# Kernel optimization log

Measured on AMD Instinct MI355X. Metric: run time of the kernel, lower is better.

Reference implementation:

```python
import jax, jax.numpy as jnp
import numpy as np

N_NODES = 50000
N_EDGES = 800000
IN_FEATS = 128
HIDDEN = 128
NUM_CLASSES = 47


def setup_inputs() -> dict:
    key = jax.random.key(0)
    k1, k2, k3, k4 = jax.random.split(key, 4)
    features = jax.random.normal(k1, (N_NODES, IN_FEATS), dtype=jnp.float32)
    edge_index = jax.random.randint(k2, (2, N_EDGES), 0, N_NODES, dtype=jnp.int32)
    # Glorot-style init for weights, zeros for bias (DGL GraphConv defaults)
    W1 = jax.random.normal(k3, (IN_FEATS, HIDDEN), dtype=jnp.float32) * (1.0 / np.sqrt(IN_FEATS))
    b1 = jnp.zeros((HIDDEN,), dtype=jnp.float32)
    W2 = jax.random.normal(k4, (HIDDEN, NUM_CLASSES), dtype=jnp.float32) * (1.0 / np.sqrt(HIDDEN))
    b2 = jnp.zeros((NUM_CLASSES,), dtype=jnp.float32)
    return {"features": features, "edge_index": edge_index,
            "W1": W1, "b1": b1, "W2": W2, "b2": b2}


def _graph_conv(x, W, b, src, dst, norm_src, norm_dst, n_nodes):
    # DGL GraphConv, norm='both': D_dst^{-1/2} A D_src^{-1/2} (X W) + b
    h = (x * norm_src[:, None]) @ W            # transform before aggregation
    agg = jax.ops.segment_sum(h[src], dst, num_segments=n_nodes)
    return agg * norm_dst[:, None] + b


def reference(features, edge_index, W1, b1, W2, b2):
    src, dst = edge_index[0], edge_index[1]
    n = features.shape[0]
    ones = jnp.ones((src.shape[0],), dtype=features.dtype)
    deg_out = jax.ops.segment_sum(ones, src, num_segments=n)
    deg_in = jax.ops.segment_sum(ones, dst, num_segments=n)
    norm_src = jax.lax.rsqrt(jnp.clip(deg_out, 1.0))   # d_out^{-1/2}, clamp >= 1
    norm_dst = jax.lax.rsqrt(jnp.clip(deg_in, 1.0))    # d_in^{-1/2}, clamp >= 1

    h = _graph_conv(features, W1, b1, src, dst, norm_src, norm_dst, n)
    h = jax.nn.relu(h)
    out = _graph_conv(h, W2, b2, src, dst, norm_src, norm_dst, n)
    return out
```

## Files before the change

kernel.cpp:

```cpp
#include <hip/hip_runtime.h>
#include <hip/hip_fp16.h>

#define N_NODES 50000
#define N_EDGES 800000
#define IN_F 128
#define HID 128
#define NCLS 47
#define H2S 48
#define W2C 64
#define NCH 196
#define NB 128
#define CHUNK 6250
#define SB 16
#define SCHUNK 50000
#define PDW 12500
#define G1B 196
#define G1ROWS 256
#define G2ROWS 128


typedef _Float16 f16x8 __attribute__((ext_vector_type(8)));
typedef float f32x4 __attribute__((ext_vector_type(4)));

struct __align__(8)  h2x2 { __half2 a, b; };
struct __align__(16) h2x4 { __half2 a, b, c, d; };

__global__ __launch_bounds__(256) void prep_kernel(const float* __restrict__ W1,
                                                   const float* __restrict__ W2,
                                                   __half* __restrict__ W1Th,
                                                   __half* __restrict__ W1Tl,
                                                   __half* __restrict__ W2Th,
                                                   __half* __restrict__ W2Tl) {
    const int b = blockIdx.x, t = threadIdx.x;
    if (b < 32) {
        const int i0 = b * 512;
        for (int i2 = i0 + t; i2 < i0 + 512; i2 += 256) {
            int cc = i2 >> 7, k = i2 & 127;
            float w = W1[k * HID + cc];
            __half hv = __float2half_rn(w);
            W1Th[i2] = hv;
            W1Tl[i2] = __float2half_rn(w - __half2float(hv));
        }
    } else {
        const int i0 = (b - 32) * 512;
        for (int i2 = i0 + t; i2 < i0 + 512; i2 += 256) {
            int cc = i2 >> 7, k = i2 & 127;
            float w = (cc < NCLS) ? W2[k * NCLS + cc] : 0.f;
            __half hv = __float2half_rn(w);
            W2Th[i2] = hv;
            W2Tl[i2] = __float2half_rn(w - __half2float(hv));
        }
    }
}

__global__ __launch_bounds__(512) void hist_gemm1_kernel(const int* __restrict__ ei,
        unsigned int* __restrict__ Pdst, unsigned int* __restrict__ Psrc,
        const float* __restrict__ X, const __half* __restrict__ W1Th,
        const __half* __restrict__ W1Tl, __half* __restrict__ H1h) {
    __shared__ unsigned int h[PDW];
    const int t = threadIdx.x;
    if (blockIdx.x >= G1B) {
        const int hb = blockIdx.x - G1B;
        const bool is_src = hb >= NB;
        const int chunk = is_src ? (hb - NB) : hb;
        const int* ids = is_src ? ei : ei + N_EDGES;
        const int cnt = is_src ? SCHUNK : CHUNK;
        uint2* h2 = (uint2*)h;
        for (int j = t; j < PDW / 2; j += 512) h2[j] = make_uint2(0u, 0u);
        __syncthreads();
        const int e0 = chunk * cnt;
        const int2* e2p = (const int2*)(ids + e0);
        for (int k = t; k < cnt / 2; k += 512) {
            int2 v2 = e2p[k];
            atomicAdd(&h[v2.x >> 2], 1u << ((v2.x & 3) * 8));
            atomicAdd(&h[v2.y >> 2], 1u << ((v2.y & 3) * 8));
        }
        __syncthreads();
        unsigned int* P = (is_src ? Psrc : Pdst) + (size_t)chunk * PDW;
        uint2* P2 = (uint2*)P;
        for (int j = t; j < PDW / 2; j += 512) P2[j] = h2[j];
    } else {
        const int lane = t & 63;
        const int wv = t >> 6;
        const int r16 = lane & 15;
        const int kg = lane >> 4;
        const int row0 = blockIdx.x * G1ROWS + wv * 32;
        f32x4 acc[2][8] = {};
#pragma unroll
        for (int s = 0; s < 4; ++s) {
            const int k0 = 32 * s + 8 * kg;
            f16x8 ah[2], al[2];
#pragma unroll
            for (int rt = 0; rt < 2; ++rt) {
                int row = row0 + rt * 16 + r16;
                int rc = row < N_NODES ? row : N_NODES - 1;
                const float4 x0 = *(const float4*)&X[(size_t)rc * IN_F + k0];
                const float4 x1 = *(const float4*)&X[(size_t)rc * IN_F + k0 + 4];
                const float xv[8] = {x0.x, x0.y, x0.z, x0.w,
                                     x1.x, x1.y, x1.z, x1.w};
#pragma unroll
                for (int j = 0; j < 8; ++j) {
                    _Float16 hv = (_Float16)xv[j];
                    ah[rt][j] = hv;
                    al[rt][j] = (_Float16)(xv[j] - (float)hv);
                }
            }
#pragma unroll
            for (int tt = 0; tt < 8; ++tt) {
                const f16x8 bh = *(const f16x8*)&W1Th[(16 * tt + r16) * IN_F + k0];
                const f16x8 bl = *(const f16x8*)&W1Tl[(16 * tt + r16) * IN_F + k0];
#pragma unroll
                for (int rt = 0; rt < 2; ++rt) {
                    acc[rt][tt] = __builtin_amdgcn_mfma_f32_16x16x32_f16(
                        ah[rt], bh, acc[rt][tt], 0, 0, 0);
                    acc[rt][tt] = __builtin_amdgcn_mfma_f32_16x16x32_f16(
                        al[rt], bh, acc[rt][tt], 0, 0, 0);
                    acc[rt][tt] = __builtin_amdgcn_mfma_f32_16x16x32_f16(
                        ah[rt], bl, acc[rt][tt], 0, 0, 0);
                }
            }
        }
#pragma unroll
        for (int rt = 0; rt < 2; ++rt)
#pragma unroll
            for (int j = 0; j < 4; ++j) {
                const int row = row0 + rt * 16 + 4 * kg + j;
                if (row < N_NODES) {
#pragma unroll
                    for (int tt = 0; tt < 8; ++tt)
                        H1h[(size_t)row * HID + 16 * tt + r16] =
                            __float2half_rn(acc[rt][tt][j]);
                }
            }
    }
}

__global__ __launch_bounds__(256) void reduce_kernel(unsigned int* __restrict__ Pdst,
                                                     const unsigned int* __restrict__ Psrc,
                                                     int* __restrict__ cnt_in,
                                                     float* __restrict__ norm_src,
                                                     float* __restrict__ norm_dst,
                                                     int* __restrict__ chunk_sums) {
    __shared__ int sm[256];
    const int t = threadIdx.x;
    const int j = blockIdx.x * 256 + t;
    int tot = 0;
    if (j < PDW) {
        unsigned int run = 0;
#pragma unroll 8
        for (int b = 0; b < NB; ++b) {
            unsigned int v = Pdst[(size_t)b * PDW + j];
            Pdst[(size_t)b * PDW + j] = run;
            run += v;
        }
        int n0 = run & 0xff, n1 = (run >> 8) & 0xff;
        int n2 = (run >> 16) & 0xff, n3 = (run >> 24) & 0xff;
        *(int4*)&cnt_in[4 * j] = make_int4(n0, n1, n2, n3);
        *(float4*)&norm_dst[4 * j] = make_float4(
            rsqrtf(fmaxf((float)n0, 1.0f)), rsqrtf(fmaxf((float)n1, 1.0f)),
            rsqrtf(fmaxf((float)n2, 1.0f)), rsqrtf(fmaxf((float)n3, 1.0f)));
        tot = n0 + n1 + n2 + n3;
        unsigned int rs = 0;
#pragma unroll
        for (int b = 0; b < SB; ++b) rs += Psrc[(size_t)b * PDW + j];
        int s0 = rs & 0xff, s1 = (rs >> 8) & 0xff;
        int s2 = (rs >> 16) & 0xff, s3 = (rs >> 24) & 0xff;
        *(float4*)&norm_src[4 * j] = make_float4(
            rsqrtf(fmaxf((float)s0, 1.0f)), rsqrtf(fmaxf((float)s1, 1.0f)),
            rsqrtf(fmaxf((float)s2, 1.0f)), rsqrtf(fmaxf((float)s3, 1.0f)));
    }
    sm[t] = tot;
    __syncthreads();
    const int g = t & 63;
    for (int off = 32; off > 0; off >>= 1) {
        if (g < off) sm[t] += sm[t + off];
        __syncthreads();
    }
    if (g == 0) chunk_sums[blockIdx.x * 4 + (t >> 6)] = sm[t];
}

__global__ __launch_bounds__(256) void scan3_kernel(const int* __restrict__ cnt_in,
                                                    const int* __restrict__ chunk_sums,
                                                    int* __restrict__ offsets) {
    __shared__ int sm[256];
    const int t = threadIdx.x;
    int v = (t < NCH) ? chunk_sums[t] : 0;
    sm[t] = v;
    __syncthreads();
    for (int off = 1; off < 256; off <<= 1) {
        int u = (t >= off) ? sm[t - off] : 0;
        __syncthreads();
        sm[t] += u;
        __syncthreads();
    }
    const int basev = (blockIdx.x == 0) ? 0 : sm[blockIdx.x - 1];
    __syncthreads();
    const int idx = blockIdx.x * 256 + t;
    int c = (idx < N_NODES) ? cnt_in[idx] : 0;
    sm[t] = c;
    __syncthreads();
    for (int off = 1; off < 256; off <<= 1) {
        int u = (t >= off) ? sm[t - off] : 0;
        __syncthreads();
        sm[t] += u;
        __syncthreads();
    }
    if (idx < N_NODES) offsets[idx] = basev + sm[t] - c;
    if (blockIdx.x == 0 && t == 0) offsets[N_NODES] = N_EDGES;
}

__global__ __launch_bounds__(512) void fill_kernel(const int* __restrict__ src,
        const int* __restrict__ dst, const int* __restrict__ offsets,
        const unsigned int* __restrict__ Pdst, int* __restrict__ csr_src) {
    __shared__ __align__(16) unsigned int cur[PDW];
    const int t = threadIdx.x;
    const int chunk = blockIdx.x;
    uint2* c2 = (uint2*)cur;
    for (int j = t; j < PDW / 2; j += 512) c2[j] = make_uint2(0u, 0u);
    __syncthreads();
    const unsigned int* base = Pdst + (size_t)chunk * PDW;
    const int e0 = chunk * CHUNK;
    const int2* d2p = (const int2*)(dst + e0);
    const int2* s2p = (const int2*)(src + e0);
    for (int k = t; k < CHUNK / 2; k += 512) {
        int2 d2 = d2p[k];
        int2 s2 = s2p[k];
        {
            const int d = d2.x;
            const int sh = (d & 3) * 8;
            const unsigned int bw = base[d >> 2];
            const int off = offsets[d];
            unsigned int old = atomicAdd(&cur[d >> 2], 1u << sh);
            csr_src[off + (int)((bw >> sh) & 0xffu) + (int)((old >> sh) & 0xffu)] = s2.x;
        }
        {
            const int d = d2.y;
            const int sh = (d & 3) * 8;
            const unsigned int bw = base[d >> 2];
            const int off = offsets[d];
            unsigned int old = atomicAdd(&cur[d >> 2], 1u << sh);
            csr_src[off + (int)((bw >> sh) & 0xffu) + (int)((old >> sh) & 0xffu)] = s2.y;
        }
    }
}

__global__ __launch_bounds__(256) void gather1_kernel(const __half* __restrict__ H1h,
        const int* __restrict__ offsets, const int* __restrict__ csr_src,
        const float* __restrict__ b1, const float* __restrict__ norm_src,
        const float* __restrict__ norm_dst, __half* __restrict__ Hrelu16) {
    const int lane = threadIdx.x & 63;
    const int q = lane >> 4;
    const int fl = lane & 15;
    const int row = blockIdx.x * 4 + (threadIdx.x >> 6);
    const int beg = offsets[row], end = offsets[row + 1];
    float a0 = 0.f, a1 = 0.f, a2 = 0.f, a3 = 0.f;
    float a4 = 0.f, a5 = 0.f, a6 = 0.f, a7 = 0.f;
    for (int base = beg; base < end; base += 64) {
        int idx = 0;
        float nsv = 0.f;
        if (base + lane < end) {
            idx = csr_src[base + lane];
            nsv = norm_src[idx];
        }
        const int cnt = min(end - base, 64);
        for (int j = 0; j < cnt; j += 16) {
            int e0 = j + q, e1 = j + 4 + q, e2 = j + 8 + q, e3 = j + 12 + q;
            int s0 = __shfl(idx, e0);  float n0 = __shfl(nsv, e0);
            int s1 = __shfl(idx, e1);  float n1 = __shfl(nsv, e1);
            int s2 = __shfl(idx, e2);  float n2 = __shfl(nsv, e2);
            int s3 = __shfl(idx, e3);  float n3 = __shfl(nsv, e3);
            h2x4 v0 = *(const h2x4*)&H1h[(size_t)s0 * HID + 8 * fl];
            h2x4 v1 = *(const h2x4*)&H1h[(size_t)s1 * HID + 8 * fl];
            h2x4 v2 = *(const h2x4*)&H1h[(size_t)s2 * HID + 8 * fl];
            h2x4 v3 = *(const h2x4*)&H1h[(size_t)s3 * HID + 8 * fl];
            float2 f;
            f = __half22float2(v0.a); a0 = fmaf(f.x, n0, a0); a1 = fmaf(f.y, n0, a1);
            f = __half22float2(v0.b); a2 = fmaf(f.x, n0, a2); a3 = fmaf(f.y, n0, a3);
            f = __half22float2(v0.c); a4 = fmaf(f.x, n0, a4); a5 = fmaf(f.y, n0, a5);
            f = __half22float2(v0.d); a6 = fmaf(f.x, n0, a6); a7 = fmaf(f.y, n0, a7);
            f = __half22float2(v1.a); a0 = fmaf(f.x, n1, a0); a1 = fmaf(f.y, n1, a1);
            f = __half22float2(v1.b); a2 = fmaf(f.x, n1, a2); a3 = fmaf(f.y, n1, a3);
            f = __half22float2(v1.c); a4 = fmaf(f.x, n1, a4); a5 = fmaf(f.y, n1, a5);
            f = __half22float2(v1.d); a6 = fmaf(f.x, n1, a6); a7 = fmaf(f.y, n1, a7);
            f = __half22float2(v2.a); a0 = fmaf(f.x, n2, a0); a1 = fmaf(f.y, n2, a1);
            f = __half22float2(v2.b); a2 = fmaf(f.x, n2, a2); a3 = fmaf(f.y, n2, a3);
            f = __half22float2(v2.c); a4 = fmaf(f.x, n2, a4); a5 = fmaf(f.y, n2, a5);
            f = __half22float2(v2.d); a6 = fmaf(f.x, n2, a6); a7 = fmaf(f.y, n2, a7);
            f = __half22float2(v3.a); a0 = fmaf(f.x, n3, a0); a1 = fmaf(f.y, n3, a1);
            f = __half22float2(v3.b); a2 = fmaf(f.x, n3, a2); a3 = fmaf(f.y, n3, a3);
            f = __half22float2(v3.c); a4 = fmaf(f.x, n3, a4); a5 = fmaf(f.y, n3, a5);
            f = __half22float2(v3.d); a6 = fmaf(f.x, n3, a6); a7 = fmaf(f.y, n3, a7);
        }
    }
    a0 += __shfl_xor(a0, 16); a1 += __shfl_xor(a1, 16);
    a2 += __shfl_xor(a2, 16); a3 += __shfl_xor(a3, 16);
    a4 += __shfl_xor(a4, 16); a5 += __shfl_xor(a5, 16);
    a6 += __shfl_xor(a6, 16); a7 += __shfl_xor(a7, 16);
    a0 += __shfl_xor(a0, 32); a1 += __shfl_xor(a1, 32);
    a2 += __shfl_xor(a2, 32); a3 += __shfl_xor(a3, 32);
    a4 += __shfl_xor(a4, 32); a5 += __shfl_xor(a5, 32);
    a6 += __shfl_xor(a6, 32); a7 += __shfl_xor(a7, 32);
    if (lane < 16) {
        float nd = norm_dst[row], ns = norm_src[row];
        float4 bA = *(const float4*)&b1[8 * fl];
        float4 bB = *(const float4*)&b1[8 * fl + 4];
        float o0 = fmaxf(fmaf(a0, nd, bA.x), 0.f) * ns;
        float o1 = fmaxf(fmaf(a1, nd, bA.y), 0.f) * ns;
        float o2 = fmaxf(fmaf(a2, nd, bA.z), 0.f) * ns;
        float o3 = fmaxf(fmaf(a3, nd, bA.w), 0.f) * ns;
        float o4 = fmaxf(fmaf(a4, nd, bB.x), 0.f) * ns;
        float o5 = fmaxf(fmaf(a5, nd, bB.y), 0.f) * ns;
        float o6 = fmaxf(fmaf(a6, nd, bB.z), 0.f) * ns;
        float o7 = fmaxf(fmaf(a7, nd, bB.w), 0.f) * ns;
        h2x4 p = {__floats2half2_rn(o0, o1), __floats2half2_rn(o2, o3),
                  __floats2half2_rn(o4, o5), __floats2half2_rn(o6, o7)};
        *(h2x4*)&Hrelu16[(size_t)row * HID + 8 * fl] = p;
    }
}

__global__ __launch_bounds__(256) void gemm2_kernel(const __half* __restrict__ Hrelu16,
                                                    const __half* __restrict__ W2Th,
                                                    const __half* __restrict__ W2Tl,
                                                    __half* __restrict__ H2h) {
    const int lane = threadIdx.x & 63;
    const int wv = threadIdx.x >> 6;
    const int r16 = lane & 15;
    const int kg = lane >> 4;
    const int row0 = blockIdx.x * G2ROWS + wv * 32;
    f32x4 acc[2][3] = {};
#pragma unroll
    for (int s = 0; s < 4; ++s) {
        const int k0 = 32 * s + 8 * kg;
        f16x8 a[2];
#pragma unroll
        for (int rt = 0; rt < 2; ++rt) {
            int row = row0 + rt * 16 + r16;
            int rc = row < N_NODES ? row : N_NODES - 1;
            a[rt] = *(const f16x8*)&Hrelu16[(size_t)rc * HID + k0];
        }
#pragma unroll
        for (int tt = 0; tt < 3; ++tt) {
            const f16x8 bh = *(const f16x8*)&W2Th[(16 * tt + r16) * HID + k0];
            const f16x8 bl = *(const f16x8*)&W2Tl[(16 * tt + r16) * HID + k0];
#pragma unroll
            for (int rt = 0; rt < 2; ++rt) {
                acc[rt][tt] = __builtin_amdgcn_mfma_f32_16x16x32_f16(
                    a[rt], bh, acc[rt][tt], 0, 0, 0);
                acc[rt][tt] = __builtin_amdgcn_mfma_f32_16x16x32_f16(
                    a[rt], bl, acc[rt][tt], 0, 0, 0);
            }
        }
    }
#pragma unroll
    for (int rt = 0; rt < 2; ++rt)
#pragma unroll
        for (int j = 0; j < 4; ++j) {
            const int row = row0 + rt * 16 + 4 * kg + j;
            if (row < N_NODES) {
#pragma unroll
                for (int tt = 0; tt < 3; ++tt)
                    H2h[(size_t)row * H2S + 16 * tt + r16] =
                        __float2half_rn(acc[rt][tt][j]);
            }
        }
}

__global__ __launch_bounds__(256) void gather2_kernel(const __half* __restrict__ H2h,
        const int* __restrict__ offsets, const int* __restrict__ csr_src,
        const float* __restrict__ b2, const float* __restrict__ norm_dst,
        float* __restrict__ out) {
    const int lane = threadIdx.x & 63;
    const int row = blockIdx.x * 4 + (threadIdx.x >> 6);
    const int beg = offsets[row], end = offsets[row + 1];
    const int cl = min(lane, H2S - 1);
    float acc = 0.f;
    for (int base = beg; base < end; base += 64) {
        int idx = 0;
        float wv = 0.f;
        if (base + lane < end) {
            idx = csr_src[base + lane];
            wv = 1.f;
        }
        const int cnt = min(end - base, 64);
        for (int j = 0; j < cnt; j += 4) {
            int s0 = __shfl(idx, j);     float w0 = __shfl(wv, j);
            int s1 = __shfl(idx, j + 1); float w1 = __shfl(wv, j + 1);
            int s2 = __shfl(idx, j + 2); float w2 = __shfl(wv, j + 2);
            int s3 = __shfl(idx, j + 3); float w3 = __shfl(wv, j + 3);
            float f0 = __half2float(H2h[(size_t)s0 * H2S + cl]);
            float f1 = __half2float(H2h[(size_t)s1 * H2S + cl]);
            float f2 = __half2float(H2h[(size_t)s2 * H2S + cl]);
            float f3 = __half2float(H2h[(size_t)s3 * H2S + cl]);
            acc = fmaf(f0, w0, acc);
            acc = fmaf(f1, w1, acc);
            acc = fmaf(f2, w2, acc);
            acc = fmaf(f3, w3, acc);
        }
    }
    if (lane < NCLS) out[(size_t)row * NCLS + lane] = acc * norm_dst[row] + b2[lane];
}

extern "C" void kernel_launch(void* const* d_in, const int* in_sizes, int n_in,
                              void* d_out, int out_size, void* d_ws, size_t ws_size,
                              hipStream_t stream) {
    const float* X  = (const float*)d_in[0];
    const int*   ei = (const int*)d_in[1];
    const float* W1 = (const float*)d_in[2];
    const float* b1 = (const float*)d_in[3];
    const float* W2 = (const float*)d_in[4];
    const float* b2 = (const float*)d_in[5];
    float* out = (float*)d_out;

    const int* src = ei;
    const int* dst = ei + N_EDGES;

    char* w = (char*)d_ws;
    auto alloc = [&](size_t bytes) {
        char* p = w;
        w += (bytes + 255) & ~(size_t)255;
        return p;
    };
    float*  norm_src   = (float*)alloc(N_NODES * 4);
    float*  norm_dst   = (float*)alloc(N_NODES * 4);
    int*    cnt_in     = (int*)alloc(N_NODES * 4);
    int*    offsets    = (int*)alloc((N_NODES + 1) * 4);
    int*    csr_src    = (int*)alloc((size_t)N_EDGES * 4);
    int*    chunk_sums = (int*)alloc(NCH * 4);
    __half* W1Th       = (__half*)alloc((size_t)IN_F * HID * 2);
    __half* W1Tl       = (__half*)alloc((size_t)IN_F * HID * 2);
    __half* W2Th       = (__half*)alloc((size_t)W2C * HID * 2);
    __half* W2Tl       = (__half*)alloc((size_t)W2C * HID * 2);
    __half* H1h        = (__half*)alloc((size_t)N_NODES * HID * 2);
    __half* Hrelu16    = (__half*)alloc((size_t)N_NODES * HID * 2);
    __half* H2h        = (__half*)alloc((size_t)N_NODES * H2S * 2);
    unsigned int* Pdst = (unsigned int*)alloc((size_t)NB * PDW * 4);
    unsigned int* Psrc = (unsigned int*)alloc((size_t)SB * PDW * 4);

    const int g2_blocks = (N_NODES + G2ROWS - 1) / G2ROWS;
    prep_kernel<<<48, 256, 0, stream>>>(W1, W2, W1Th, W1Tl, W2Th, W2Tl);
    hist_gemm1_kernel<<<G1B + NB + SB, 512, 0, stream>>>(ei, Pdst, Psrc,
                                                         X, W1Th, W1Tl, H1h);
    reduce_kernel<<<(PDW + 255) / 256, 256, 0, stream>>>(Pdst, Psrc, cnt_in,
                                                         norm_src, norm_dst, chunk_sums);
    scan3_kernel<<<NCH, 256, 0, stream>>>(cnt_in, chunk_sums, offsets);
    fill_kernel<<<NB, 512, 0, stream>>>(src, dst, offsets, Pdst, csr_src);
    gather1_kernel<<<N_NODES / 4, 256, 0, stream>>>(H1h, offsets, csr_src, b1,
                                                    norm_src, norm_dst, Hrelu16);
    gemm2_kernel<<<g2_blocks, 256, 0, stream>>>(Hrelu16, W2Th, W2Tl, H2h);
    gather2_kernel<<<N_NODES / 4, 256, 0, stream>>>(H2h, offsets, csr_src, b2,
                                                    norm_dst, out);
}
```

Before: 202.8 us.

## Move GEMM1 into fill kernel, prescale rows by norm_src, merge weight prep into histogram

The weight-split prep is folded into the histogram kernel as extra blocks, which removes one launch. GEMM1 moves out of the histogram kernel and runs alongside the CSR fill. Because norm_src is known by then, GEMM1 scales each output row by it, so gather1 no longer loads norm_src per edge. GEMM1 tiles shrink to 128 rows with one 16-row tile per wave, and the source histogram is split into more chunks. The risk is that GEMM1 now comes after the reduce and scan stages, so it no longer overlaps with the histogram and lengthens the dependent chain.

Result: slower. 216.9 us (+7.0%).

```diff
diff --git a/kernel.cpp b/kernel.cpp
--- a/kernel.cpp
+++ b/kernel.cpp
@@ -11,11 +11,11 @@
 #define NCH 196
 #define NB 128
 #define CHUNK 6250
-#define SB 16
-#define SCHUNK 50000
+#define SB 32
+#define SCHUNK 25000
 #define PDW 12500
-#define G1B 196
-#define G1ROWS 256
+#define G1ROWS 128
+#define G1B 391
 #define G2ROWS 128
 
 
@@ -25,44 +25,16 @@
 struct __align__(8)  h2x2 { __half2 a, b; };
 struct __align__(16) h2x4 { __half2 a, b, c, d; };
 
-__global__ __launch_bounds__(256) void prep_kernel(const float* __restrict__ W1,
-                                                   const float* __restrict__ W2,
-                                                   __half* __restrict__ W1Th,
-                                                   __half* __restrict__ W1Tl,
-                                                   __half* __restrict__ W2Th,
-                                                   __half* __restrict__ W2Tl) {
-    const int b = blockIdx.x, t = threadIdx.x;
-    if (b < 32) {
-        const int i0 = b * 512;
-        for (int i2 = i0 + t; i2 < i0 + 512; i2 += 256) {
-            int cc = i2 >> 7, k = i2 & 127;
-            float w = W1[k * HID + cc];
-            __half hv = __float2half_rn(w);
-            W1Th[i2] = hv;
-            W1Tl[i2] = __float2half_rn(w - __half2float(hv));
-        }
-    } else {
-        const int i0 = (b - 32) * 512;
-        for (int i2 = i0 + t; i2 < i0 + 512; i2 += 256) {
-            int cc = i2 >> 7, k = i2 & 127;
-            float w = (cc < NCLS) ? W2[k * NCLS + cc] : 0.f;
-            __half hv = __float2half_rn(w);
-            W2Th[i2] = hv;
-            W2Tl[i2] = __float2half_rn(w - __half2float(hv));
-        }
-    }
-}
-
-__global__ __launch_bounds__(512) void hist_gemm1_kernel(const int* __restrict__ ei,
+__global__ __launch_bounds__(512) void hist_prep_kernel(const int* __restrict__ ei,
         unsigned int* __restrict__ Pdst, unsigned int* __restrict__ Psrc,
-        const float* __restrict__ X, const __half* __restrict__ W1Th,
-        const __half* __restrict__ W1Tl, __half* __restrict__ H1h) {
+        const float* __restrict__ W1, const float* __restrict__ W2,
+        __half* __restrict__ W1Th, __half* __restrict__ W1Tl,
+        __half* __restrict__ W2Th, __half* __restrict__ W2Tl) {
     __shared__ unsigned int h[PDW];
     const int t = threadIdx.x;
-    if (blockIdx.x >= G1B) {
-        const int hb = blockIdx.x - G1B;
-        const bool is_src = hb >= NB;
-        const int chunk = is_src ? (hb - NB) : hb;
+    if (blockIdx.x < NB + SB) {
+        const bool is_src = blockIdx.x >= NB;
+        const int chunk = is_src ? (blockIdx.x - NB) : blockIdx.x;
         const int* ids = is_src ? ei : ei + N_EDGES;
         const int cnt = is_src ? SCHUNK : CHUNK;
         uint2* h2 = (uint2*)h;
@@ -80,58 +52,22 @@
         uint2* P2 = (uint2*)P;
         for (int j = t; j < PDW / 2; j += 512) P2[j] = h2[j];
     } else {
-        const int lane = t & 63;
-        const int wv = t >> 6;
-        const int r16 = lane & 15;
-        const int kg = lane >> 4;
-        const int row0 = blockIdx.x * G1ROWS + wv * 32;
-        f32x4 acc[2][8] = {};
-#pragma unroll
-        for (int s = 0; s < 4; ++s) {
-            const int k0 = 32 * s + 8 * kg;
-            f16x8 ah[2], al[2];
-#pragma unroll
-            for (int rt = 0; rt < 2; ++rt) {
-                int row = row0 + rt * 16 + r16;
-                int rc = row < N_NODES ? row : N_NODES - 1;
-                const float4 x0 = *(const float4*)&X[(size_t)rc * IN_F + k0];
-                const float4 x1 = *(const float4*)&X[(size_t)rc * IN_F + k0 + 4];
-                const float xv[8] = {x0.x, x0.y, x0.z, x0.w,
-                                     x1.x, x1.y, x1.z, x1.w};
-#pragma unroll
-                for (int j = 0; j < 8; ++j) {
-                    _Float16 hv = (_Float16)xv[j];
-                    ah[rt][j] = hv;
-                    al[rt][j] = (_Float16)(xv[j] - (float)hv);
-                }
-            }
-#pragma unroll
-            for (int tt = 0; tt < 8; ++tt) {
-                const f16x8 bh = *(const f16x8*)&W1Th[(16 * tt + r16) * IN_F + k0];
-                const f16x8 bl = *(const f16x8*)&W1Tl[(16 * tt + r16) * IN_F + k0];
-#pragma unroll
-                for (int rt = 0; rt < 2; ++rt) {
-                    acc[rt][tt] = __builtin_amdgcn_mfma_f32_16x16x32_f16(
-                        ah[rt], bh, acc[rt][tt], 0, 0, 0);
-                    acc[rt][tt] = __builtin_amdgcn_mfma_f32_16x16x32_f16(
-                        al[rt], bh, acc[rt][tt], 0, 0, 0);
-                    acc[rt][tt] = __builtin_amdgcn_mfma_f32_16x16x32_f16(
-                        ah[rt], bl, acc[rt][tt], 0, 0, 0);
-                }
-            }
-        }
-#pragma unroll
-        for (int rt = 0; rt < 2; ++rt)
-#pragma unroll
-            for (int j = 0; j < 4; ++j) {
-                const int row = row0 + rt * 16 + 4 * kg + j;
-                if (row < N_NODES) {
-#pragma unroll
-                    for (int tt = 0; tt < 8; ++tt)
-                        H1h[(size_t)row * HID + 16 * tt + r16] =
-                            __float2half_rn(acc[rt][tt][j]);
-                }
-            }
+        const int pj = blockIdx.x - (NB + SB);
+        if (pj < 32) {
+            const int i2 = pj * 512 + t;
+            int cc = i2 >> 7, k = i2 & 127;
+            float w = W1[k * HID + cc];
+            __half hv = __float2half_rn(w);
+            W1Th[i2] = hv;
+            W1Tl[i2] = __float2half_rn(w - __half2float(hv));
+        } else {
+            const int i2 = (pj - 32) * 512 + t;
+            int cc = i2 >> 7, k = i2 & 127;
+            float w = (cc < NCLS) ? W2[k * NCLS + cc] : 0.f;
+            __half hv = __float2half_rn(w);
+            W2Th[i2] = hv;
+            W2Tl[i2] = __float2half_rn(w - __half2float(hv));
+        }
     }
 }
 
@@ -161,7 +97,7 @@
             rsqrtf(fmaxf((float)n2, 1.0f)), rsqrtf(fmaxf((float)n3, 1.0f)));
         tot = n0 + n1 + n2 + n3;
         unsigned int rs = 0;
-#pragma unroll
+#pragma unroll 8
         for (int b = 0; b < SB; ++b) rs += Psrc[(size_t)b * PDW + j];
         int s0 = rs & 0xff, s1 = (rs >> 8) & 0xff;
         int s2 = (rs >> 16) & 0xff, s3 = (rs >> 24) & 0xff;
@@ -209,37 +145,91 @@
     if (blockIdx.x == 0 && t == 0) offsets[N_NODES] = N_EDGES;
 }
 
-__global__ __launch_bounds__(512) void fill_kernel(const int* __restrict__ src,
+__global__ __launch_bounds__(512) void fill_gemm1_kernel(const int* __restrict__ src,
         const int* __restrict__ dst, const int* __restrict__ offsets,
-        const unsigned int* __restrict__ Pdst, int* __restrict__ csr_src) {
+        const unsigned int* __restrict__ Pdst, int* __restrict__ csr_src,
+        const float* __restrict__ X, const float* __restrict__ norm_src,
+        const __half* __restrict__ W1Th, const __half* __restrict__ W1Tl,
+        __half* __restrict__ H1h) {
     __shared__ __align__(16) unsigned int cur[PDW];
     const int t = threadIdx.x;
-    const int chunk = blockIdx.x;
-    uint2* c2 = (uint2*)cur;
-    for (int j = t; j < PDW / 2; j += 512) c2[j] = make_uint2(0u, 0u);
-    __syncthreads();
-    const unsigned int* base = Pdst + (size_t)chunk * PDW;
-    const int e0 = chunk * CHUNK;
-    const int2* d2p = (const int2*)(dst + e0);
-    const int2* s2p = (const int2*)(src + e0);
-    for (int k = t; k < CHUNK / 2; k += 512) {
-        int2 d2 = d2p[k];
-        int2 s2 = s2p[k];
-        {
-            const int d = d2.x;
-            const int sh = (d & 3) * 8;
-            const unsigned int bw = base[d >> 2];
-            const int off = offsets[d];
-            unsigned int old = atomicAdd(&cur[d >> 2], 1u << sh);
-            csr_src[off + (int)((bw >> sh) & 0xffu) + (int)((old >> sh) & 0xffu)] = s2.x;
-        }
-        {
-            const int d = d2.y;
-            const int sh = (d & 3) * 8;
-            const unsigned int bw = base[d >> 2];
-            const int off = offsets[d];
-            unsigned int old = atomicAdd(&cur[d >> 2], 1u << sh);
-            csr_src[off + (int)((bw >> sh) & 0xffu) + (int)((old >> sh) & 0xffu)] = s2.y;
+    if (blockIdx.x < NB) {
+        const int chunk = blockIdx.x;
+        uint2* c2 = (uint2*)cur;
+        for (int j = t; j < PDW / 2; j += 512) c2[j] = make_uint2(0u, 0u);
+        __syncthreads();
+        const unsigned int* base = Pdst + (size_t)chunk * PDW;
+        const int e0 = chunk * CHUNK;
+        const int2* d2p = (const int2*)(dst + e0);
+        const int2* s2p = (const int2*)(src + e0);
+        for (int k = t; k < CHUNK / 2; k += 512) {
+            int2 d2 = d2p[k];
+            int2 s2 = s2p[k];
+            {
+                const int d = d2.x;
+                const int sh = (d & 3) * 8;
+                const unsigned int bw = base[d >> 2];
+                const int off = offsets[d];
+                unsigned int old = atomicAdd(&cur[d >> 2], 1u << sh);
+                csr_src[off + (int)((bw >> sh) & 0xffu) + (int)((old >> sh) & 0xffu)] = s2.x;
+            }
+            {
+                const int d = d2.y;
+                const int sh = (d & 3) * 8;
+                const unsigned int bw = base[d >> 2];
+                const int off = offsets[d];
+                unsigned int old = atomicAdd(&cur[d >> 2], 1u << sh);
+                csr_src[off + (int)((bw >> sh) & 0xffu) + (int)((old >> sh) & 0xffu)] = s2.y;
+            }
+        }
+    } else {
+        const int lane = t & 63;
+        const int wv = t >> 6;
+        const int r16 = lane & 15;
+        const int kg = lane >> 4;
+        const int row0 = (blockIdx.x - NB) * G1ROWS + wv * 16;
+        const int ar = row0 + r16;
+        const int arc = ar < N_NODES ? ar : N_NODES - 1;
+        const float* xp = &X[(size_t)arc * IN_F + 8 * kg];
+        float4 xr[8];
+#pragma unroll
+        for (int s = 0; s < 4; ++s) {
+            xr[2 * s]     = *(const float4*)(xp + 32 * s);
+            xr[2 * s + 1] = *(const float4*)(xp + 32 * s + 4);
+        }
+        f32x4 acc[8] = {};
+#pragma unroll
+        for (int s = 0; s < 4; ++s) {
+            const int k0 = 32 * s + 8 * kg;
+            const float xv[8] = {xr[2 * s].x, xr[2 * s].y, xr[2 * s].z, xr[2 * s].w,
+                                 xr[2 * s + 1].x, xr[2 * s + 1].y,
+                                 xr[2 * s + 1].z, xr[2 * s + 1].w};
+            f16x8 ah, al;
+#pragma unroll
+            for (int j = 0; j < 8; ++j) {
+                _Float16 hv = (_Float16)xv[j];
+                ah[j] = hv;
+                al[j] = (_Float16)(xv[j] - (float)hv);
+            }
+#pragma unroll
+            for (int tt = 0; tt < 8; ++tt) {
+                const f16x8 bh = *(const f16x8*)&W1Th[(16 * tt + r16) * IN_F + k0];
+                const f16x8 bl = *(const f16x8*)&W1Tl[(16 * tt + r16) * IN_F + k0];
+                acc[tt] = __builtin_amdgcn_mfma_f32_16x16x32_f16(ah, bh, acc[tt], 0, 0, 0);
+                acc[tt] = __builtin_amdgcn_mfma_f32_16x16x32_f16(al, bh, acc[tt], 0, 0, 0);
+                acc[tt] = __builtin_amdgcn_mfma_f32_16x16x32_f16(ah, bl, acc[tt], 0, 0, 0);
+            }
+        }
+#pragma unroll
+        for (int j = 0; j < 4; ++j) {
+            const int row = row0 + 4 * kg + j;
+            if (row < N_NODES) {
+                const float nsr = norm_src[row];
+#pragma unroll
+                for (int tt = 0; tt < 8; ++tt)
+                    H1h[(size_t)row * HID + 16 * tt + r16] =
+                        __float2half_rn(acc[tt][j] * nsr);
+            }
         }
     }
 }
@@ -257,18 +247,18 @@
     float a4 = 0.f, a5 = 0.f, a6 = 0.f, a7 = 0.f;
     for (int base = beg; base < end; base += 64) {
         int idx = 0;
-        float nsv = 0.f;
+        float mv = 0.f;
         if (base + lane < end) {
             idx = csr_src[base + lane];
-            nsv = norm_src[idx];
+            mv = 1.f;
         }
         const int cnt = min(end - base, 64);
         for (int j = 0; j < cnt; j += 16) {
             int e0 = j + q, e1 = j + 4 + q, e2 = j + 8 + q, e3 = j + 12 + q;
-            int s0 = __shfl(idx, e0);  float n0 = __shfl(nsv, e0);
-            int s1 = __shfl(idx, e1);  float n1 = __shfl(nsv, e1);
-            int s2 = __shfl(idx, e2);  float n2 = __shfl(nsv, e2);
-            int s3 = __shfl(idx, e3);  float n3 = __shfl(nsv, e3);
+            int s0 = __shfl(idx, e0);  float n0 = __shfl(mv, e0);
+            int s1 = __shfl(idx, e1);  float n1 = __shfl(mv, e1);
+            int s2 = __shfl(idx, e2);  float n2 = __shfl(mv, e2);
+            int s3 = __shfl(idx, e3);  float n3 = __shfl(mv, e3);
             h2x4 v0 = *(const h2x4*)&H1h[(size_t)s0 * HID + 8 * fl];
             h2x4 v1 = *(const h2x4*)&H1h[(size_t)s1 * HID + 8 * fl];
             h2x4 v2 = *(const h2x4*)&H1h[(size_t)s2 * HID + 8 * fl];
@@ -437,13 +427,14 @@
     unsigned int* Psrc = (unsigned int*)alloc((size_t)SB * PDW * 4);
 
     const int g2_blocks = (N_NODES + G2ROWS - 1) / G2ROWS;
-    prep_kernel<<<48, 256, 0, stream>>>(W1, W2, W1Th, W1Tl, W2Th, W2Tl);
-    hist_gemm1_kernel<<<G1B + NB + SB, 512, 0, stream>>>(ei, Pdst, Psrc,
-                                                         X, W1Th, W1Tl, H1h);
+    hist_prep_kernel<<<NB + SB + 48, 512, 0, stream>>>(ei, Pdst, Psrc, W1, W2,
+                                                       W1Th, W1Tl, W2Th, W2Tl);
     reduce_kernel<<<(PDW + 255) / 256, 256, 0, stream>>>(Pdst, Psrc, cnt_in,
                                                          norm_src, norm_dst, chunk_sums);
     scan3_kernel<<<NCH, 256, 0, stream>>>(cnt_in, chunk_sums, offsets);
-    fill_kernel<<<NB, 512, 0, stream>>>(src, dst, offsets, Pdst, csr_src);
+    fill_gemm1_kernel<<<NB + G1B, 512, 0, stream>>>(src, dst, offsets, Pdst,
+                                                    csr_src, X, norm_src,
+                                                    W1Th, W1Tl, H1h);
     gather1_kernel<<<N_NODES / 4, 256, 0, stream>>>(H1h, offsets, csr_src, b1,
                                                     norm_src, norm_dst, Hrelu16);
     gemm2_kernel<<<g2_blocks, 256, 0, stream>>>(Hrelu16, W2Th, W2Tl, H2h);
```
